# Kernel tuning notes

Hardware: AMD Instinct MI355X
Metric: run time of the kernel (lower is better)

## Reference

```python
import jax, jax.numpy as jnp
import numpy as np

B, QS, KS, E, H = 2, 2048, 2048, 2048, 16
D = E // H  # head_dim = 128
EPS = 1e-6


def setup_inputs() -> dict:
    key = jax.random.key(0)
    ks = jax.random.split(key, 11)
    scale_in = 1.0 / np.sqrt(E)  # lecun_normal fan_in = E
    scale_out = 1.0 / np.sqrt(E)  # fan_in for out proj = H*D = E
    return {
        "q": jax.random.normal(ks[0], (B, QS, E), jnp.float32),
        "kv": jax.random.normal(ks[1], (B, KS, E), jnp.float32),
        "q_pos": jax.random.normal(ks[2], (B, QS, E), jnp.float32),
        "kv_pos": jax.random.normal(ks[3], (B, KS, E), jnp.float32),
        "mask": jax.random.bernoulli(ks[4], 0.5, (B, QS, KS)),
        "wq": jax.random.normal(ks[5], (E, H, D), jnp.float32) * scale_in,
        "wk": jax.random.normal(ks[6], (E, H, D), jnp.float32) * scale_in,
        "wv": jax.random.normal(ks[7], (E, H, D), jnp.float32) * scale_in,
        "q_ln_scale": jnp.ones((D,), jnp.float32),
        "k_ln_scale": jnp.ones((D,), jnp.float32),
        "wo": jax.random.normal(ks[8], (H, D, E), jnp.float32) * scale_out,
    }


def _layernorm_no_bias(x, scale):
    # flax LayerNorm over last axis, use_bias=False, epsilon=1e-6
    mu = jnp.mean(x, axis=-1, keepdims=True)
    var = jnp.mean(jnp.square(x - mu), axis=-1, keepdims=True)
    return (x - mu) * jax.lax.rsqrt(var + EPS) * scale


def reference(q, kv, q_pos, kv_pos, mask, wq, wk, wv, q_ln_scale, k_ln_scale, wo):
    dtype = q.dtype
    qi = q + q_pos          # [b, qs, e]
    ki = kv + kv_pos        # [b, ks, e]
    vi = kv
    # QKV projections (DenseGeneral, no bias) -> [b, s, h, d]
    qh = jnp.einsum('bqe,ehd->bqhd', qi, wq)
    kh = jnp.einsum('bke,ehd->bkhd', ki, wk)
    vh = jnp.einsum('bke,ehd->bkhd', vi, wv)
    # normalize_qk: LayerNorm (no bias) on query/key over head_dim
    qh = _layernorm_no_bias(qh, q_ln_scale)
    kh = _layernorm_no_bias(kh, k_ln_scale)
    # scaled dot-product with float32 logits
    qh = qh / jnp.sqrt(jnp.asarray(D, dtype))
    logits = jnp.einsum('bqhd,bkhd->bhqk', qh, kh,
                        preferred_element_type=jnp.float32)
    big_neg = jnp.finfo(jnp.float32).min
    logits = jnp.where(mask[:, None, :, :], logits, big_neg)
    attn = jax.nn.softmax(logits, axis=-1).astype(dtype)  # [b,h,q,k]
    out = jnp.einsum('bhqk,bkhd->bqhd', attn, vh)
    # output projection (DenseGeneral over (h,d), no bias)
    return jnp.einsum('bqhd,hde->bqe', out, wo)
```

## Files before the change

kernel.cpp:

```cpp
#include <hip/hip_runtime.h>
#include <hip/hip_bf16.h>


typedef __attribute__((ext_vector_type(8))) __bf16 bf16x8;
typedef __attribute__((ext_vector_type(4))) float f32x4;
typedef __attribute__((ext_vector_type(8))) unsigned short ushort8;
typedef __attribute__((ext_vector_type(4))) unsigned short ushort4v;
typedef __attribute__((ext_vector_type(4))) unsigned uint4v;
typedef __attribute__((ext_vector_type(4))) float float4v;

#define MFMA16(a, b, c) __builtin_amdgcn_mfma_f32_16x16x32_bf16((a), (b), (c), 0, 0, 0)

__device__ __forceinline__ unsigned short f2bf(float f) {
  unsigned u = __builtin_bit_cast(unsigned, f);
  u += 0x7fffu + ((u >> 16) & 1u);
  return (unsigned short)(u >> 16);
}

__device__ __forceinline__ unsigned pkbf(float lo, float hi) {
  unsigned d;
  asm("v_cvt_pk_bf16_f32 %0, %1, %2" : "=v"(d) : "v"(lo), "v"(hi));
  return d;
}

__device__ __forceinline__ float max3f(float a, float b, float c) {
  float d;
  asm("v_max3_f32 %0, %1, %2, %3" : "=v"(d) : "v"(a), "v"(b), "v"(c));
  return d;
}

__device__ __forceinline__ float exp2a(float x) {
  float d;
  asm("v_exp_f32 %0, %1" : "=v"(d) : "v"(x));
  return d;
}

__device__ __forceinline__ void gload_lds16(const void* g, void* l) {
  __builtin_amdgcn_global_load_lds(
      (const __attribute__((address_space(1))) void*)g,
      (__attribute__((address_space(3))) void*)l, 16, 0, 0);
}

__global__ __launch_bounds__(256) void k_cvt(const float4v* __restrict__ x,
                                             const float4v* __restrict__ y,
                                             ushort4v* __restrict__ o, int n4) {
  int i = blockIdx.x * 256 + threadIdx.x;
  if (i >= n4) return;
  float4v a = x[i];
  if (y) { float4v b = y[i]; a = a + b; }
  ushort4v r;
  r[0] = f2bf(a[0]); r[1] = f2bf(a[1]); r[2] = f2bf(a[2]); r[3] = f2bf(a[3]);
  o[i] = r;
}

__global__ __launch_bounds__(256) void k_cvt2(const float4v* __restrict__ x,
                                              const float4v* __restrict__ y,
                                              ushort4v* __restrict__ oa,
                                              ushort4v* __restrict__ ob, int n4) {
  int i = blockIdx.x * 256 + threadIdx.x;
  if (i >= n4) return;
  float4v a = x[i];
  float4v s = a + y[i];
  ushort4v ra, rb;
  ra[0] = f2bf(s[0]); ra[1] = f2bf(s[1]); ra[2] = f2bf(s[2]); ra[3] = f2bf(s[3]);
  rb[0] = f2bf(a[0]); rb[1] = f2bf(a[1]); rb[2] = f2bf(a[2]); rb[3] = f2bf(a[3]);
  oa[i] = ra; ob[i] = rb;
}

__global__ __launch_bounds__(256) void k_tr(const float* __restrict__ s0, const float* __restrict__ s1,
                                            const float* __restrict__ s2, const float* __restrict__ s3,
                                            unsigned short* __restrict__ d0, unsigned short* __restrict__ d1,
                                            unsigned short* __restrict__ d2, unsigned short* __restrict__ d3) {
  __shared__ float t[32][33];
  const float* S; unsigned short* D;
  switch (blockIdx.z) {
    case 0: S = s0; D = d0; break;
    case 1: S = s1; D = d1; break;
    case 2: S = s2; D = d2; break;
    default: S = s3; D = d3; break;
  }
  int x = threadIdx.x & 31, y = threadIdx.x >> 5;
  int r0 = blockIdx.y * 32, c0 = blockIdx.x * 32;
#pragma unroll
  for (int i = 0; i < 4; ++i) t[y + 8 * i][x] = S[(size_t)(r0 + y + 8 * i) * 2048 + c0 + x];
  __syncthreads();
#pragma unroll
  for (int i = 0; i < 4; ++i)
    D[(size_t)(c0 + y + 8 * i) * 2048 + r0 + x] = f2bf(t[x][y + 8 * i]);
}

__global__ __launch_bounds__(256) void k_mask(const int* __restrict__ m,
                                              unsigned long long* __restrict__ out) {
  int i = blockIdx.x * 256 + threadIdx.x;
  unsigned long long b = __ballot(m[i] != 0);
  if ((threadIdx.x & 63) == 0) out[i >> 6] = b;
}

__global__ __launch_bounds__(256) void k_trv(const unsigned short* __restrict__ Vh,
                                             unsigned short* __restrict__ Vt) {
  __shared__ unsigned short t[64][72];
  int bh = blockIdx.z;
  int s0 = blockIdx.x * 64, d0 = blockIdx.y * 64;
  size_t base = (size_t)bh * 2048 * 128;
  int row = threadIdx.x >> 2, c16 = (threadIdx.x & 3) * 16;
  {
    const unsigned short* src = Vh + base + (size_t)(s0 + row) * 128 + d0 + c16;
    ushort8 a0 = *(const ushort8*)src;
    ushort8 a1 = *(const ushort8*)(src + 8);
#pragma unroll
    for (int e = 0; e < 8; ++e) {
      t[c16 + e][row] = a0[e];
      t[c16 + 8 + e][row] = a1[e];
    }
  }
  __syncthreads();
  {
    unsigned short* dst = Vt + base + (size_t)(d0 + row) * 2048 + s0 + c16;
    *(ushort8*)dst = *(const ushort8*)&t[row][c16];
    *(ushort8*)(dst + 8) = *(const ushort8*)&t[row][c16 + 8];
  }
}

template <int MODE>
__global__ __launch_bounds__(256) void k_gemm(const unsigned short* __restrict__ A,
                                              const unsigned short* __restrict__ Bt,
                                              void* __restrict__ Cv,
                                              const float* __restrict__ lnsc) {
  constexpr int K = 2048;
  __shared__ __attribute__((aligned(16))) unsigned short sA[128 * 64];
  __shared__ __attribute__((aligned(16))) unsigned short sB[128 * 64];
  __shared__ float sSum[2][128];
  __shared__ float sSq[2][128];
  int tid = threadIdx.x;
  int lane = tid & 63, w = tid >> 6;
  int wr = w >> 1, wc = w & 1;
  int r15 = lane & 15, blk = lane >> 4;
  int n0 = blockIdx.x * 128, m0 = blockIdx.y * 128;
  const unsigned short* Abase = A + (size_t)m0 * K;
  const unsigned short* Bbase = Bt + (size_t)n0 * K;
  f32x4 acc[4][4] = {};

  for (int kt = 0; kt < K; kt += 64) {
#pragma unroll
    for (int i = 0; i < 4; ++i) {
      int c = i * 256 + tid;
      int row = c >> 3, cc = c & 7;
      gload_lds16(Abase + (size_t)row * K + kt + ((cc ^ (row & 7)) * 8), &sA[c * 8]);
    }
#pragma unroll
    for (int i = 0; i < 4; ++i) {
      int c = i * 256 + tid;
      int row = c >> 3, cc = c & 7;
      gload_lds16(Bbase + (size_t)row * K + kt + ((cc ^ (row & 7)) * 8), &sB[c * 8]);
    }
    __syncthreads();
#pragma unroll
    for (int kk = 0; kk < 2; ++kk) {
      bf16x8 av[4], bv[4];
#pragma unroll
      for (int i = 0; i < 4; ++i) {
        int row = wr * 64 + i * 16 + r15;
        av[i] = *(const bf16x8*)&sA[row * 64 + (((kk * 4 + blk) ^ (row & 7)) * 8)];
      }
#pragma unroll
      for (int j = 0; j < 4; ++j) {
        int row = wc * 64 + j * 16 + r15;
        bv[j] = *(const bf16x8*)&sB[row * 64 + (((kk * 4 + blk) ^ (row & 7)) * 8)];
      }
#pragma unroll
      for (int i = 0; i < 4; ++i)
#pragma unroll
        for (int j = 0; j < 4; ++j) acc[i][j] = MFMA16(av[i], bv[j], acc[i][j]);
    }
    __syncthreads();
  }

  if constexpr (MODE == 3) {
    float* C = (float*)Cv;
#pragma unroll
    for (int i = 0; i < 4; ++i)
#pragma unroll
      for (int r = 0; r < 4; ++r)
#pragma unroll
        for (int j = 0; j < 4; ++j) {
          int rowl = wr * 64 + i * 16 + blk * 4 + r;
          int coll = wc * 64 + j * 16 + r15;
          C[(size_t)(m0 + rowl) * 2048 + n0 + coll] = acc[i][j][r];
        }
    return;
  } else {
    if constexpr (MODE == 1 || MODE == 2) {
#pragma unroll
      for (int i = 0; i < 4; ++i)
#pragma unroll
        for (int r = 0; r < 4; ++r) {
          float sm = 0.f, sq = 0.f;
#pragma unroll
          for (int j = 0; j < 4; ++j) { float v = acc[i][j][r]; sm += v; sq += v * v; }
          sm += __shfl_xor(sm, 1); sq += __shfl_xor(sq, 1);
          sm += __shfl_xor(sm, 2); sq += __shfl_xor(sq, 2);
          sm += __shfl_xor(sm, 4); sq += __shfl_xor(sq, 4);
          sm += __shfl_xor(sm, 8); sq += __shfl_xor(sq, 8);
          if (r15 == 0) {
            int rowl = wr * 64 + i * 16 + blk * 4 + r;
            sSum[wc][rowl] = sm; sSq[wc][rowl] = sq;
          }
        }
      __syncthreads();
    }
    unsigned short* Hout = (unsigned short*)Cv;
    int h = blockIdx.x;
#pragma unroll
    for (int i = 0; i < 4; ++i)
#pragma unroll
      for (int r = 0; r < 4; ++r) {
        int rowl = wr * 64 + i * 16 + blk * 4 + r;
        float mean = 0.f, rstd = 1.f;
        if constexpr (MODE == 1 || MODE == 2) {
          float sm = sSum[0][rowl] + sSum[1][rowl];
          float sq = sSq[0][rowl] + sSq[1][rowl];
          mean = sm * 0.0078125f;
          float var = sq * 0.0078125f - mean * mean;
          rstd = rsqrtf(var + 1e-6f);
        }
        int rowg = m0 + rowl;
        int b = rowg >> 11, s = rowg & 2047;
        unsigned short* orow = Hout + (((size_t)b * 16 + h) * 2048 + s) * 128;
#pragma unroll
        for (int j = 0; j < 4; ++j) {
          int d = wc * 64 + j * 16 + r15;
          float v = acc[i][j][r];
          if constexpr (MODE == 1)
            v = (v - mean) * rstd * lnsc[d] * (0.08838834764831845f * 1.4426950408889634f);
          if constexpr (MODE == 2) v = (v - mean) * rstd * lnsc[d];
          orow[d] = f2bf(v);
        }
      }
  }
}

__device__ __forceinline__ void softmax_grp(const f32x4 (&st)[4], unsigned mw0, unsigned mw1,
                                            int blk, float& mv, float& ls,
                                            f32x4 (&o)[8], bf16x8& plo, bf16x8& phi) {
  unsigned mws0 = mw0 >> (blk * 8);
  unsigned mws1 = mw1 >> (blk * 8);
  float pvv[16];
#pragma unroll
  for (int t = 0; t < 16; ++t) {
    int s = t >> 2, r = t & 3;
    unsigned mws = (s & 2) ? mws1 : mws0;
    int bit = 4 * (s & 1) + r;
    pvv[t] = ((mws >> bit) & 1u) ? st[s][r] : -1e30f;
  }
  float c0 = max3f(pvv[0], pvv[1], pvv[2]);
  float c1 = max3f(pvv[3], pvv[4], pvv[5]);
  float c2 = max3f(pvv[6], pvv[7], pvv[8]);
  float c3 = max3f(pvv[9], pvv[10], pvv[11]);
  float c4 = max3f(pvv[12], pvv[13], pvv[14]);
  float cmax = fmaxf(max3f(c0, c1, c2), max3f(c3, c4, pvv[15]));
  cmax = fmaxf(cmax, __shfl_xor(cmax, 16));
  cmax = fmaxf(cmax, __shfl_xor(cmax, 32));
  if (!__all(cmax - mv <= 11.5f)) {
    float mnew = fmaxf(mv, cmax);
    float fac = exp2a(mv - mnew);
    ls *= fac;
    float fr0 = __shfl(fac, blk * 4 + 0);
    float fr1 = __shfl(fac, blk * 4 + 1);
    float fr2 = __shfl(fac, blk * 4 + 2);
    float fr3 = __shfl(fac, blk * 4 + 3);
#pragma unroll
    for (int t8 = 0; t8 < 8; ++t8) {
      o[t8][0] *= fr0; o[t8][1] *= fr1; o[t8][2] *= fr2; o[t8][3] *= fr3;
    }
    mv = mnew;
  }
#pragma unroll
  for (int t = 0; t < 16; ++t) pvv[t] = exp2a(pvv[t] - mv);
  float s0 = (pvv[0] + pvv[1]) + (pvv[2] + pvv[3]);
  float s1 = (pvv[4] + pvv[5]) + (pvv[6] + pvv[7]);
  float s2 = (pvv[8] + pvv[9]) + (pvv[10] + pvv[11]);
  float s3 = (pvv[12] + pvv[13]) + (pvv[14] + pvv[15]);
  ls += (s0 + s1) + (s2 + s3);
  uint4v w0, w1;
#pragma unroll
  for (int j = 0; j < 4; ++j) {
    w0[j] = pkbf(pvv[2 * j], pvv[2 * j + 1]);
    w1[j] = pkbf(pvv[8 + 2 * j], pvv[9 + 2 * j]);
  }
  plo = __builtin_bit_cast(bf16x8, w0);
  phi = __builtin_bit_cast(bf16x8, w1);
}

__global__ __launch_bounds__(256, 2) void k_attn(const unsigned short* __restrict__ Qh,
                                                 const unsigned short* __restrict__ Kh,
                                                 const unsigned short* __restrict__ Vt,
                                                 const unsigned* __restrict__ maskb,
                                                 unsigned short* __restrict__ O) {
  __shared__ __attribute__((aligned(16))) char smem[65536];
  int tid = threadIdx.x, w = tid >> 6;
  int lane = tid & 63;
  int r15 = lane & 15, blk = lane >> 4;
  int bh = blockIdx.y, b = bh >> 4, h = bh & 15;
  int qb = blockIdx.x * 128;
  size_t base = (size_t)bh * (2048 * 128);
  int qrow0 = qb + w * 32 + r15;
  int qrow1 = qrow0 + 16;

  bf16x8 qf0[4], qf1[4];
  {
    const unsigned short* qp0 = Qh + base + (size_t)qrow0 * 128 + blk * 8;
    const unsigned short* qp1 = Qh + base + (size_t)qrow1 * 128 + blk * 8;
#pragma unroll
    for (int kk = 0; kk < 4; ++kk) {
      qf0[kk] = *(const bf16x8*)(qp0 + kk * 32);
      qf1[kk] = *(const bf16x8*)(qp1 + kk * 32);
    }
  }
  const unsigned* mrow0 = maskb + ((size_t)b * 2048 + qrow0) * 64;
  const unsigned* mrow1 = maskb + ((size_t)b * 2048 + qrow1) * 64;

  const unsigned short* kgp[4];
  const unsigned short* vgp[4];
#pragma unroll
  for (int i = 0; i < 4; ++i) {
    int c = i * 256 + tid;
    int krow = c >> 4, kcc = c & 15;
    int key = 32 * (krow >> 5) + 8 * ((krow >> 2) & 3) + 4 * ((krow >> 4) & 1) + (krow & 3);
    kgp[i] = Kh + base + (size_t)key * 128 + ((kcc ^ (krow & 7)) * 8);
    int d = c >> 3, c8 = c & 7;
    vgp[i] = Vt + base + (size_t)d * 2048 + ((c8 ^ (d & 7)) * 8);
  }

  f32x4 o0[8] = {}, o1[8] = {};
  float m0v = -1e30f, l0 = 0.f, m1v = -1e30f, l1 = 0.f;

#pragma unroll
  for (int i = 0; i < 4; ++i) {
    int c = i * 256 + tid;
    gload_lds16(kgp[i], (unsigned short*)smem + c * 8);
    gload_lds16(vgp[i], (unsigned short*)(smem + 16384) + c * 8);
  }
  __syncthreads();

  int cur = 0;
  for (int kc = 0; kc < 2048; kc += 64) {
    if (kc + 64 < 2048) {
      char* nb = smem + ((cur ^ 1) << 15);
#pragma unroll
      for (int i = 0; i < 4; ++i) {
        int c = i * 256 + tid;
        gload_lds16(kgp[i] + (size_t)(kc + 64) * 128, (unsigned short*)nb + c * 8);
        gload_lds16(vgp[i] + (kc + 64), (unsigned short*)(nb + 16384) + c * 8);
      }
    }
    const unsigned short* sK = (const unsigned short*)(smem + (cur << 15));
    const unsigned short* sV = (const unsigned short*)(smem + (cur << 15) + 16384);

    f32x4 st0[4] = {}, st1[4] = {};
#pragma unroll
    for (int kk = 0; kk < 4; ++kk) {
      int cc = (4 * kk + blk) ^ (r15 & 7);
#pragma unroll
      for (int s = 0; s < 4; ++s) {
        bf16x8 kf = *(const bf16x8*)&sK[(16 * s + r15) * 128 + cc * 8];
        st0[s] = MFMA16(kf, qf0[kk], st0[s]);
        st1[s] = MFMA16(kf, qf1[kk], st1[s]);
      }
    }

    unsigned a0 = mrow0[kc >> 5], a1 = mrow0[(kc >> 5) + 1];
    unsigned b0 = mrow1[kc >> 5], b1 = mrow1[(kc >> 5) + 1];
    bf16x8 pf00, pf01, pf10, pf11;
    softmax_grp(st0, a0, a1, blk, m0v, l0, o0, pf00, pf01);
    softmax_grp(st1, b0, b1, blk, m1v, l1, o1, pf10, pf11);

#pragma unroll
    for (int t8 = 0; t8 < 8; ++t8) {
      int vr = t8 * 16 + r15;
      bf16x8 v0 = *(const bf16x8*)&sV[vr * 64 + ((blk ^ (r15 & 7)) * 8)];
      bf16x8 v1 = *(const bf16x8*)&sV[vr * 64 + (((4 + blk) ^ (r15 & 7)) * 8)];
      o0[t8] = MFMA16(pf00, v0, o0[t8]);
      o0[t8] = MFMA16(pf01, v1, o0[t8]);
      o1[t8] = MFMA16(pf10, v0, o1[t8]);
      o1[t8] = MFMA16(pf11, v1, o1[t8]);
    }
    __syncthreads();
    cur ^= 1;
  }

  float* sO = (float*)smem;
  {
    l0 += __shfl_xor(l0, 16); l0 += __shfl_xor(l0, 32);
    float inv = 1.f / l0;
    float ir0 = __shfl(inv, blk * 4 + 0), ir1 = __shfl(inv, blk * 4 + 1);
    float ir2 = __shfl(inv, blk * 4 + 2), ir3 = __shfl(inv, blk * 4 + 3);
#pragma unroll
    for (int t8 = 0; t8 < 8; ++t8) {
      int bi = (w * 16 + blk * 4) * 132 + t8 * 16 + r15;
      sO[bi] = o0[t8][0] * ir0;
      sO[bi + 132] = o0[t8][1] * ir1;
      sO[bi + 264] = o0[t8][2] * ir2;
      sO[bi + 396] = o0[t8][3] * ir3;
    }
  }
  __syncthreads();
  {
    int row = tid >> 2, d0 = (tid & 3) * 32;
    int grow = qb + (row >> 4) * 32 + (row & 15);
    unsigned short* op = O + (size_t)(b * 2048 + grow) * 2048 + h * 128 + d0;
#pragma unroll
    for (int g4 = 0; g4 < 4; ++g4) {
      ushort8 pk;
#pragma unroll
      for (int e = 0; e < 8; ++e) pk[e] = f2bf(sO[row * 132 + d0 + g4 * 8 + e]);
      *(ushort8*)(op + g4 * 8) = pk;
    }
  }
  __syncthreads();
  {
    l1 += __shfl_xor(l1, 16); l1 += __shfl_xor(l1, 32);
    float inv = 1.f / l1;
    float ir0 = __shfl(inv, blk * 4 + 0), ir1 = __shfl(inv, blk * 4 + 1);
    float ir2 = __shfl(inv, blk * 4 + 2), ir3 = __shfl(inv, blk * 4 + 3);
#pragma unroll
    for (int t8 = 0; t8 < 8; ++t8) {
      int bi = (w * 16 + blk * 4) * 132 + t8 * 16 + r15;
      sO[bi] = o1[t8][0] * ir0;
      sO[bi + 132] = o1[t8][1] * ir1;
      sO[bi + 264] = o1[t8][2] * ir2;
      sO[bi + 396] = o1[t8][3] * ir3;
    }
  }
  __syncthreads();
  {
    int row = tid >> 2, d0 = (tid & 3) * 32;
    int grow = qb + (row >> 4) * 32 + 16 + (row & 15);
    unsigned short* op = O + (size_t)(b * 2048 + grow) * 2048 + h * 128 + d0;
#pragma unroll
    for (int g4 = 0; g4 < 4; ++g4) {
      ushort8 pk;
#pragma unroll
      for (int e = 0; e < 8; ++e) pk[e] = f2bf(sO[row * 132 + d0 + g4 * 8 + e]);
      *(ushort8*)(op + g4 * 8) = pk;
    }
  }
}

extern "C" void kernel_launch(void* const* d_in, const int* in_sizes, int n_in,
                              void* d_out, int out_size, void* d_ws, size_t ws_size,
                              hipStream_t stream) {
  const float* q      = (const float*)d_in[0];
  const float* kv     = (const float*)d_in[1];
  const float* q_pos  = (const float*)d_in[2];
  const float* kv_pos = (const float*)d_in[3];
  const int*   mask   = (const int*)d_in[4];
  const float* wq     = (const float*)d_in[5];
  const float* wk     = (const float*)d_in[6];
  const float* wv     = (const float*)d_in[7];
  const float* qls    = (const float*)d_in[8];
  const float* kls    = (const float*)d_in[9];
  const float* wo     = (const float*)d_in[10];

  char* ws = (char*)d_ws;
  const size_t SZ_ACT = (size_t)4096 * 2048 * 2;
  const size_t SZ_W   = (size_t)2048 * 2048 * 2;
  unsigned short* a_q = (unsigned short*)(ws);
  unsigned short* a_k = (unsigned short*)(ws + SZ_ACT);
  unsigned short* a_v = (unsigned short*)(ws + 2 * SZ_ACT);
  unsigned short* Qh  = (unsigned short*)(ws + 3 * SZ_ACT);
  unsigned short* Kh  = (unsigned short*)(ws + 4 * SZ_ACT);
  unsigned short* Vh  = (unsigned short*)(ws + 5 * SZ_ACT);
  unsigned short* wqt = (unsigned short*)(ws + 6 * SZ_ACT);
  unsigned short* wkt = (unsigned short*)(ws + 6 * SZ_ACT + SZ_W);
  unsigned short* wvt = (unsigned short*)(ws + 6 * SZ_ACT + 2 * SZ_W);
  unsigned short* wot = (unsigned short*)(ws + 6 * SZ_ACT + 3 * SZ_W);
  unsigned*       mkb = (unsigned*)(ws + 6 * SZ_ACT + 4 * SZ_W);
  unsigned short* Ob  = a_q;
  unsigned short* Vtr = a_k;

  const size_t NEED = 6 * SZ_ACT + 4 * SZ_W + (size_t)2 * 2048 * 64 * 4;
  if (ws_size < NEED) return;

  k_cvt<<<8192, 256, 0, stream>>>((const float4v*)q, (const float4v*)q_pos, (ushort4v*)a_q, 2097152);
  k_cvt2<<<8192, 256, 0, stream>>>((const float4v*)kv, (const float4v*)kv_pos,
                                   (ushort4v*)a_k, (ushort4v*)a_v, 2097152);
  k_tr<<<dim3(64, 64, 4), 256, 0, stream>>>(wq, wk, wv, wo, wqt, wkt, wvt, wot);
  k_mask<<<32768, 256, 0, stream>>>(mask, (unsigned long long*)mkb);

  k_gemm<1><<<dim3(16, 32), 256, 0, stream>>>(a_q, wqt, Qh, qls);
  k_gemm<2><<<dim3(16, 32), 256, 0, stream>>>(a_k, wkt, Kh, kls);
  k_gemm<0><<<dim3(16, 32), 256, 0, stream>>>(a_v, wvt, Vh, nullptr);

  k_trv<<<dim3(32, 2, 32), 256, 0, stream>>>(Vh, Vtr);

  k_attn<<<dim3(16, 32), 256, 0, stream>>>(Qh, Kh, Vtr, mkb, Ob);

  k_gemm<3><<<dim3(16, 32), 256, 0, stream>>>(Ob, wot, d_out, nullptr);
}
```

Baseline: 353.1 us.

## Halve attention key tile to 32 and raise occupancy to four blocks per CU

The flash-attention kernel now processes 32 keys per iteration instead of 64. That halves the K/V shared-memory double buffers, the score registers and the softmax working set. The smaller footprint allows launch_bounds(256,4), so more workgroups can be resident per CU to hide latency. The cost is twice as many loop iterations, with more barriers, mask loads and online-softmax max/rescale steps per key. The K swizzle and V layout were reworked to match the narrower tile.

```diff
diff --git a/kernel.cpp b/kernel.cpp
--- a/kernel.cpp
+++ b/kernel.cpp
@@ -239,25 +239,19 @@
   }
 }
 
-__device__ __forceinline__ void softmax_grp(const f32x4 (&st)[4], unsigned mw0, unsigned mw1,
-                                            int blk, float& mv, float& ls,
-                                            f32x4 (&o)[8], bf16x8& plo, bf16x8& phi) {
-  unsigned mws0 = mw0 >> (blk * 8);
-  unsigned mws1 = mw1 >> (blk * 8);
-  float pvv[16];
-#pragma unroll
-  for (int t = 0; t < 16; ++t) {
+__device__ __forceinline__ void softmax_grp8(const f32x4 (&st)[2], unsigned mw,
+                                             int blk, float& mv, float& ls,
+                                             f32x4 (&o)[8], bf16x8& pf) {
+  unsigned mws = mw >> (blk * 8);
+  float pvv[8];
+#pragma unroll
+  for (int t = 0; t < 8; ++t) {
     int s = t >> 2, r = t & 3;
-    unsigned mws = (s & 2) ? mws1 : mws0;
-    int bit = 4 * (s & 1) + r;
-    pvv[t] = ((mws >> bit) & 1u) ? st[s][r] : -1e30f;
+    pvv[t] = ((mws >> t) & 1u) ? st[s][r] : -1e30f;
   }
   float c0 = max3f(pvv[0], pvv[1], pvv[2]);
   float c1 = max3f(pvv[3], pvv[4], pvv[5]);
-  float c2 = max3f(pvv[6], pvv[7], pvv[8]);
-  float c3 = max3f(pvv[9], pvv[10], pvv[11]);
-  float c4 = max3f(pvv[12], pvv[13], pvv[14]);
-  float cmax = fmaxf(max3f(c0, c1, c2), max3f(c3, c4, pvv[15]));
+  float cmax = max3f(c0, c1, fmaxf(pvv[6], pvv[7]));
   cmax = fmaxf(cmax, __shfl_xor(cmax, 16));
   cmax = fmaxf(cmax, __shfl_xor(cmax, 32));
   if (!__all(cmax - mv <= 11.5f)) {
@@ -275,28 +269,20 @@
     mv = mnew;
   }
 #pragma unroll
-  for (int t = 0; t < 16; ++t) pvv[t] = exp2a(pvv[t] - mv);
-  float s0 = (pvv[0] + pvv[1]) + (pvv[2] + pvv[3]);
-  float s1 = (pvv[4] + pvv[5]) + (pvv[6] + pvv[7]);
-  float s2 = (pvv[8] + pvv[9]) + (pvv[10] + pvv[11]);
-  float s3 = (pvv[12] + pvv[13]) + (pvv[14] + pvv[15]);
-  ls += (s0 + s1) + (s2 + s3);
-  uint4v w0, w1;
-#pragma unroll
-  for (int j = 0; j < 4; ++j) {
-    w0[j] = pkbf(pvv[2 * j], pvv[2 * j + 1]);
-    w1[j] = pkbf(pvv[8 + 2 * j], pvv[9 + 2 * j]);
-  }
-  plo = __builtin_bit_cast(bf16x8, w0);
-  phi = __builtin_bit_cast(bf16x8, w1);
-}
-
-__global__ __launch_bounds__(256, 2) void k_attn(const unsigned short* __restrict__ Qh,
+  for (int t = 0; t < 8; ++t) pvv[t] = exp2a(pvv[t] - mv);
+  ls += ((pvv[0] + pvv[1]) + (pvv[2] + pvv[3])) + ((pvv[4] + pvv[5]) + (pvv[6] + pvv[7]));
+  uint4v wv;
+#pragma unroll
+  for (int j = 0; j < 4; ++j) wv[j] = pkbf(pvv[2 * j], pvv[2 * j + 1]);
+  pf = __builtin_bit_cast(bf16x8, wv);
+}
+
+__global__ __launch_bounds__(256, 4) void k_attn(const unsigned short* __restrict__ Qh,
                                                  const unsigned short* __restrict__ Kh,
                                                  const unsigned short* __restrict__ Vt,
                                                  const unsigned* __restrict__ maskb,
                                                  unsigned short* __restrict__ O) {
-  __shared__ __attribute__((aligned(16))) char smem[65536];
+  __shared__ __attribute__((aligned(16))) char smem[33792];
   int tid = threadIdx.x, w = tid >> 6;
   int lane = tid & 63;
   int r15 = lane & 15, blk = lane >> 4;
@@ -319,70 +305,66 @@
   const unsigned* mrow0 = maskb + ((size_t)b * 2048 + qrow0) * 64;
   const unsigned* mrow1 = maskb + ((size_t)b * 2048 + qrow1) * 64;
 
-  const unsigned short* kgp[4];
-  const unsigned short* vgp[4];
-#pragma unroll
-  for (int i = 0; i < 4; ++i) {
+  const unsigned short* kgp[2];
+  const unsigned short* vgp[2];
+#pragma unroll
+  for (int i = 0; i < 2; ++i) {
     int c = i * 256 + tid;
-    int krow = c >> 4, kcc = c & 15;
-    int key = 32 * (krow >> 5) + 8 * ((krow >> 2) & 3) + 4 * ((krow >> 4) & 1) + (krow & 3);
-    kgp[i] = Kh + base + (size_t)key * 128 + ((kcc ^ (krow & 7)) * 8);
-    int d = c >> 3, c8 = c & 7;
-    vgp[i] = Vt + base + (size_t)d * 2048 + ((c8 ^ (d & 7)) * 8);
+    int rr = c >> 4, cc = c & 15;
+    int key = 8 * ((rr & 15) >> 2) + 4 * (rr >> 4) + (rr & 3);
+    kgp[i] = Kh + base + (size_t)key * 128 + ((cc ^ (rr & 7)) * 8);
+    int d = c >> 2, c4 = c & 3;
+    vgp[i] = Vt + base + (size_t)d * 2048 + ((c4 ^ (d & 3)) * 8);
   }
 
   f32x4 o0[8] = {}, o1[8] = {};
   float m0v = -1e30f, l0 = 0.f, m1v = -1e30f, l1 = 0.f;
 
 #pragma unroll
-  for (int i = 0; i < 4; ++i) {
+  for (int i = 0; i < 2; ++i) {
     int c = i * 256 + tid;
     gload_lds16(kgp[i], (unsigned short*)smem + c * 8);
-    gload_lds16(vgp[i], (unsigned short*)(smem + 16384) + c * 8);
+    gload_lds16(vgp[i], (unsigned short*)(smem + 8192) + c * 8);
   }
   __syncthreads();
 
   int cur = 0;
-  for (int kc = 0; kc < 2048; kc += 64) {
-    if (kc + 64 < 2048) {
-      char* nb = smem + ((cur ^ 1) << 15);
-#pragma unroll
-      for (int i = 0; i < 4; ++i) {
+  for (int kc = 0; kc < 2048; kc += 32) {
+    if (kc + 32 < 2048) {
+      char* nb = smem + ((cur ^ 1) << 14);
+#pragma unroll
+      for (int i = 0; i < 2; ++i) {
         int c = i * 256 + tid;
-        gload_lds16(kgp[i] + (size_t)(kc + 64) * 128, (unsigned short*)nb + c * 8);
-        gload_lds16(vgp[i] + (kc + 64), (unsigned short*)(nb + 16384) + c * 8);
+        gload_lds16(kgp[i] + (size_t)(kc + 32) * 128, (unsigned short*)nb + c * 8);
+        gload_lds16(vgp[i] + (kc + 32), (unsigned short*)(nb + 8192) + c * 8);
       }
     }
-    const unsigned short* sK = (const unsigned short*)(smem + (cur << 15));
-    const unsigned short* sV = (const unsigned short*)(smem + (cur << 15) + 16384);
-
-    f32x4 st0[4] = {}, st1[4] = {};
+    const unsigned short* sK = (const unsigned short*)(smem + (cur << 14));
+    const unsigned short* sV = (const unsigned short*)(smem + (cur << 14) + 8192);
+
+    f32x4 st0[2] = {}, st1[2] = {};
 #pragma unroll
     for (int kk = 0; kk < 4; ++kk) {
       int cc = (4 * kk + blk) ^ (r15 & 7);
 #pragma unroll
-      for (int s = 0; s < 4; ++s) {
+      for (int s = 0; s < 2; ++s) {
         bf16x8 kf = *(const bf16x8*)&sK[(16 * s + r15) * 128 + cc * 8];
         st0[s] = MFMA16(kf, qf0[kk], st0[s]);
         st1[s] = MFMA16(kf, qf1[kk], st1[s]);
       }
     }
 
-    unsigned a0 = mrow0[kc >> 5], a1 = mrow0[(kc >> 5) + 1];
-    unsigned b0 = mrow1[kc >> 5], b1 = mrow1[(kc >> 5) + 1];
-    bf16x8 pf00, pf01, pf10, pf11;
-    softmax_grp(st0, a0, a1, blk, m0v, l0, o0, pf00, pf01);
-    softmax_grp(st1, b0, b1, blk, m1v, l1, o1, pf10, pf11);
+    unsigned a0 = mrow0[kc >> 5], b0 = mrow1[kc >> 5];
+    bf16x8 pf0, pf1;
+    softmax_grp8(st0, a0, blk, m0v, l0, o0, pf0);
+    softmax_grp8(st1, b0, blk, m1v, l1, o1, pf1);
 
 #pragma unroll
     for (int t8 = 0; t8 < 8; ++t8) {
       int vr = t8 * 16 + r15;
-      bf16x8 v0 = *(const bf16x8*)&sV[vr * 64 + ((blk ^ (r15 & 7)) * 8)];
-      bf16x8 v1 = *(const bf16x8*)&sV[vr * 64 + (((4 + blk) ^ (r15 & 7)) * 8)];
-      o0[t8] = MFMA16(pf00, v0, o0[t8]);
-      o0[t8] = MFMA16(pf01, v1, o0[t8]);
-      o1[t8] = MFMA16(pf10, v0, o1[t8]);
-      o1[t8] = MFMA16(pf11, v1, o1[t8]);
+      bf16x8 v = *(const bf16x8*)&sV[vr * 32 + ((blk ^ (r15 & 3)) * 8)];
+      o0[t8] = MFMA16(pf0, v, o0[t8]);
+      o1[t8] = MFMA16(pf1, v, o1[t8]);
     }
     __syncthreads();
     cur ^= 1;
```

Result: slower. 491.8 us (+39.3%).

## Split attention query tile across 8 waves with one 16-row group each

Applied to the files above, without the earlier changes.

The attention kernel moves from 4 waves each handling two 16-row query groups to 8 waves (512 threads) each handling one group, keeping the same 128-query tile and shared K/V staging. This halves per-wave accumulator and score registers and raises the number of waves available to hide MFMA and LDS latency. In exchange, the K/V tile loaded into LDS is shared by more waves with fewer MFMAs per LDS fragment read per wave. The epilogue becomes two passes through shared memory, one per half of the waves.

```diff
diff --git a/kernel.cpp b/kernel.cpp
--- a/kernel.cpp
+++ b/kernel.cpp
@@ -291,7 +291,7 @@
   phi = __builtin_bit_cast(bf16x8, w1);
 }
 
-__global__ __launch_bounds__(256, 2) void k_attn(const unsigned short* __restrict__ Qh,
+__global__ __launch_bounds__(512, 4) void k_attn(const unsigned short* __restrict__ Qh,
                                                  const unsigned short* __restrict__ Kh,
                                                  const unsigned short* __restrict__ Vt,
                                                  const unsigned* __restrict__ maskb,
@@ -303,40 +303,34 @@
   int bh = blockIdx.y, b = bh >> 4, h = bh & 15;
   int qb = blockIdx.x * 128;
   size_t base = (size_t)bh * (2048 * 128);
-  int qrow0 = qb + w * 32 + r15;
-  int qrow1 = qrow0 + 16;
-
-  bf16x8 qf0[4], qf1[4];
+  int qrow = qb + w * 16 + r15;
+
+  bf16x8 qf[4];
   {
-    const unsigned short* qp0 = Qh + base + (size_t)qrow0 * 128 + blk * 8;
-    const unsigned short* qp1 = Qh + base + (size_t)qrow1 * 128 + blk * 8;
-#pragma unroll
-    for (int kk = 0; kk < 4; ++kk) {
-      qf0[kk] = *(const bf16x8*)(qp0 + kk * 32);
-      qf1[kk] = *(const bf16x8*)(qp1 + kk * 32);
-    }
-  }
-  const unsigned* mrow0 = maskb + ((size_t)b * 2048 + qrow0) * 64;
-  const unsigned* mrow1 = maskb + ((size_t)b * 2048 + qrow1) * 64;
-
-  const unsigned short* kgp[4];
-  const unsigned short* vgp[4];
-#pragma unroll
-  for (int i = 0; i < 4; ++i) {
-    int c = i * 256 + tid;
-    int krow = c >> 4, kcc = c & 15;
-    int key = 32 * (krow >> 5) + 8 * ((krow >> 2) & 3) + 4 * ((krow >> 4) & 1) + (krow & 3);
-    kgp[i] = Kh + base + (size_t)key * 128 + ((kcc ^ (krow & 7)) * 8);
+    const unsigned short* qp = Qh + base + (size_t)qrow * 128 + blk * 8;
+#pragma unroll
+    for (int kk = 0; kk < 4; ++kk) qf[kk] = *(const bf16x8*)(qp + kk * 32);
+  }
+  const unsigned* mrow = maskb + ((size_t)b * 2048 + qrow) * 64;
+
+  const unsigned short* kgp[2];
+  const unsigned short* vgp[2];
+#pragma unroll
+  for (int i = 0; i < 2; ++i) {
+    int c = i * 512 + tid;
+    int rr = c >> 4, cc = c & 15;
+    int key = 32 * (rr >> 5) + 8 * ((rr >> 2) & 3) + 4 * ((rr >> 4) & 1) + (rr & 3);
+    kgp[i] = Kh + base + (size_t)key * 128 + ((cc ^ (rr & 7)) * 8);
     int d = c >> 3, c8 = c & 7;
     vgp[i] = Vt + base + (size_t)d * 2048 + ((c8 ^ (d & 7)) * 8);
   }
 
-  f32x4 o0[8] = {}, o1[8] = {};
-  float m0v = -1e30f, l0 = 0.f, m1v = -1e30f, l1 = 0.f;
-
-#pragma unroll
-  for (int i = 0; i < 4; ++i) {
-    int c = i * 256 + tid;
+  f32x4 o[8] = {};
+  float mv = -1e30f, ls = 0.f;
+
+#pragma unroll
+  for (int i = 0; i < 2; ++i) {
+    int c = i * 512 + tid;
     gload_lds16(kgp[i], (unsigned short*)smem + c * 8);
     gload_lds16(vgp[i], (unsigned short*)(smem + 16384) + c * 8);
   }
@@ -347,8 +341,8 @@
     if (kc + 64 < 2048) {
       char* nb = smem + ((cur ^ 1) << 15);
 #pragma unroll
-      for (int i = 0; i < 4; ++i) {
-        int c = i * 256 + tid;
+      for (int i = 0; i < 2; ++i) {
+        int c = i * 512 + tid;
         gload_lds16(kgp[i] + (size_t)(kc + 64) * 128, (unsigned short*)nb + c * 8);
         gload_lds16(vgp[i] + (kc + 64), (unsigned short*)(nb + 16384) + c * 8);
       }
@@ -356,93 +350,69 @@
     const unsigned short* sK = (const unsigned short*)(smem + (cur << 15));
     const unsigned short* sV = (const unsigned short*)(smem + (cur << 15) + 16384);
 
-    f32x4 st0[4] = {}, st1[4] = {};
+    f32x4 st[4] = {};
 #pragma unroll
     for (int kk = 0; kk < 4; ++kk) {
       int cc = (4 * kk + blk) ^ (r15 & 7);
 #pragma unroll
       for (int s = 0; s < 4; ++s) {
         bf16x8 kf = *(const bf16x8*)&sK[(16 * s + r15) * 128 + cc * 8];
-        st0[s] = MFMA16(kf, qf0[kk], st0[s]);
-        st1[s] = MFMA16(kf, qf1[kk], st1[s]);
-      }
-    }
-
-    unsigned a0 = mrow0[kc >> 5], a1 = mrow0[(kc >> 5) + 1];
-    unsigned b0 = mrow1[kc >> 5], b1 = mrow1[(kc >> 5) + 1];
-    bf16x8 pf00, pf01, pf10, pf11;
-    softmax_grp(st0, a0, a1, blk, m0v, l0, o0, pf00, pf01);
-    softmax_grp(st1, b0, b1, blk, m1v, l1, o1, pf10, pf11);
+        st[s] = MFMA16(kf, qf[kk], st[s]);
+      }
+    }
+
+    unsigned mw0 = mrow[kc >> 5], mw1 = mrow[(kc >> 5) + 1];
+    bf16x8 pf0, pf1;
+    softmax_grp(st, mw0, mw1, blk, mv, ls, o, pf0, pf1);
 
 #pragma unroll
     for (int t8 = 0; t8 < 8; ++t8) {
       int vr = t8 * 16 + r15;
       bf16x8 v0 = *(const bf16x8*)&sV[vr * 64 + ((blk ^ (r15 & 7)) * 8)];
       bf16x8 v1 = *(const bf16x8*)&sV[vr * 64 + (((4 + blk) ^ (r15 & 7)) * 8)];
-      o0[t8] = MFMA16(pf00, v0, o0[t8]);
-      o0[t8] = MFMA16(pf01, v1, o0[t8]);
-      o1[t8] = MFMA16(pf10, v0, o1[t8]);
-      o1[t8] = MFMA16(pf11, v1, o1[t8]);
+      o[t8] = MFMA16(pf0, v0, o[t8]);
+      o[t8] = MFMA16(pf1, v1, o[t8]);
     }
     __syncthreads();
     cur ^= 1;
   }
 
+  ls += __shfl_xor(ls, 16);
+  ls += __shfl_xor(ls, 32);
+  float inv = 1.f / ls;
+  float ir0 = __shfl(inv, blk * 4 + 0), ir1 = __shfl(inv, blk * 4 + 1);
+  float ir2 = __shfl(inv, blk * 4 + 2), ir3 = __shfl(inv, blk * 4 + 3);
+
   float* sO = (float*)smem;
-  {
-    l0 += __shfl_xor(l0, 16); l0 += __shfl_xor(l0, 32);
-    float inv = 1.f / l0;
-    float ir0 = __shfl(inv, blk * 4 + 0), ir1 = __shfl(inv, blk * 4 + 1);
-    float ir2 = __shfl(inv, blk * 4 + 2), ir3 = __shfl(inv, blk * 4 + 3);
-#pragma unroll
-    for (int t8 = 0; t8 < 8; ++t8) {
-      int bi = (w * 16 + blk * 4) * 132 + t8 * 16 + r15;
-      sO[bi] = o0[t8][0] * ir0;
-      sO[bi + 132] = o0[t8][1] * ir1;
-      sO[bi + 264] = o0[t8][2] * ir2;
-      sO[bi + 396] = o0[t8][3] * ir3;
-    }
-  }
   __syncthreads();
-  {
-    int row = tid >> 2, d0 = (tid & 3) * 32;
-    int grow = qb + (row >> 4) * 32 + (row & 15);
-    unsigned short* op = O + (size_t)(b * 2048 + grow) * 2048 + h * 128 + d0;
-#pragma unroll
-    for (int g4 = 0; g4 < 4; ++g4) {
-      ushort8 pk;
-#pragma unroll
-      for (int e = 0; e < 8; ++e) pk[e] = f2bf(sO[row * 132 + d0 + g4 * 8 + e]);
-      *(ushort8*)(op + g4 * 8) = pk;
-    }
-  }
-  __syncthreads();
-  {
-    l1 += __shfl_xor(l1, 16); l1 += __shfl_xor(l1, 32);
-    float inv = 1.f / l1;
-    float ir0 = __shfl(inv, blk * 4 + 0), ir1 = __shfl(inv, blk * 4 + 1);
-    float ir2 = __shfl(inv, blk * 4 + 2), ir3 = __shfl(inv, blk * 4 + 3);
-#pragma unroll
-    for (int t8 = 0; t8 < 8; ++t8) {
-      int bi = (w * 16 + blk * 4) * 132 + t8 * 16 + r15;
-      sO[bi] = o1[t8][0] * ir0;
-      sO[bi + 132] = o1[t8][1] * ir1;
-      sO[bi + 264] = o1[t8][2] * ir2;
-      sO[bi + 396] = o1[t8][3] * ir3;
-    }
-  }
-  __syncthreads();
-  {
-    int row = tid >> 2, d0 = (tid & 3) * 32;
-    int grow = qb + (row >> 4) * 32 + 16 + (row & 15);
-    unsigned short* op = O + (size_t)(b * 2048 + grow) * 2048 + h * 128 + d0;
-#pragma unroll
-    for (int g4 = 0; g4 < 4; ++g4) {
-      ushort8 pk;
-#pragma unroll
-      for (int e = 0; e < 8; ++e) pk[e] = f2bf(sO[row * 132 + d0 + g4 * 8 + e]);
-      *(ushort8*)(op + g4 * 8) = pk;
-    }
+#pragma unroll
+  for (int pass = 0; pass < 2; ++pass) {
+    if ((w >> 2) == pass) {
+      int wl = w & 3;
+#pragma unroll
+      for (int t8 = 0; t8 < 8; ++t8) {
+        int bi = (wl * 16 + blk * 4) * 132 + t8 * 16 + r15;
+        sO[bi] = o[t8][0] * ir0;
+        sO[bi + 132] = o[t8][1] * ir1;
+        sO[bi + 264] = o[t8][2] * ir2;
+        sO[bi + 396] = o[t8][3] * ir3;
+      }
+    }
+    __syncthreads();
+    {
+      int row = tid >> 3, d0 = (tid & 7) * 16;
+      int grow = qb + pass * 64 + row;
+      unsigned short* op = O + (size_t)(b * 2048 + grow) * 2048 + h * 128 + d0;
+      ushort8 pk0, pk1;
+#pragma unroll
+      for (int e = 0; e < 8; ++e) {
+        pk0[e] = f2bf(sO[row * 132 + d0 + e]);
+        pk1[e] = f2bf(sO[row * 132 + d0 + 8 + e]);
+      }
+      *(ushort8*)op = pk0;
+      *(ushort8*)(op + 8) = pk1;
+    }
+    __syncthreads();
   }
 }
 
@@ -493,7 +463,7 @@
 
   k_trv<<<dim3(32, 2, 32), 256, 0, stream>>>(Vh, Vtr);
 
-  k_attn<<<dim3(16, 32), 256, 0, stream>>>(Qh, Kh, Vtr, mkb, Ob);
+  k_attn<<<dim3(16, 32), 512, 0, stream>>>(Qh, Kh, Vtr, mkb, Ob);
 
   k_gemm<3><<<dim3(16, 32), 256, 0, stream>>>(Ob, wot, d_out, nullptr);
 }
```

Measured after the change: 353.3 us. No clear change (+0.1%).
